# Kernel tuning notes

Measured on AMD Instinct MI355X. Metric: run time of the kernel, lower is better.

## Reference

```python
import jax, jax.numpy as jnp
import numpy as np

LN_EPS = 1e-3   # keras LayerNormalization default epsilon
STAB = 1e-3     # performer relu-kernel numerical stabilizer
N = 2           # number of blocks per branch


def layer_norm(x, g, b):
    m = jnp.mean(x, axis=-1, keepdims=True)
    v = jnp.mean(jnp.square(x - m), axis=-1, keepdims=True)
    return (x - m) * jax.lax.rsqrt(v + LN_EPS) * g + b


def favor(q_in, kv_in, Wq, Wk, Wv, Wo):
    # Performer FAVOR attention, relu kernel features (google-research fast_attention,
    # projection_matrix_type=None). q/k/v head projections have no bias.
    q = jnp.einsum('bld,dhm->blhm', q_in, Wq)
    k = jnp.einsum('bsd,dhm->bshm', kv_in, Wk)
    v = jnp.einsum('bsd,dhm->bshm', kv_in, Wv)
    norm = q.shape[-1] ** -0.25  # 1/sqrt(sqrt(head_dim))
    qp = jax.nn.relu(q * norm) + STAB
    kp = jax.nn.relu(k * norm) + STAB
    kv = jnp.einsum('bshm,bshd->bhmd', kp, v)
    num = jnp.einsum('blhm,bhmd->blhd', qp, kv)
    den = jnp.einsum('blhm,bhm->blh', qp, kp.sum(axis=1))
    out = num / den[..., None]
    return jnp.einsum('blhd,hde->ble', out, Wo)


def forward(obj_inputs, road_inputs,
            rg_dense_W, rg_dense_b, rg_qkv_W, rg_qkv_b,
            rg_Wq, rg_Wk, rg_Wv, rg_Wo, rg_ln_g, rg_ln_b, rg_fc_W, rg_fc_b,
            rg_out_W, rg_out_b,
            dense_W, dense_b, pos_emb,
            Wq, Wk, Wv, Wo, ln_g, ln_b, fc_W, fc_b):
    rgH = rg_dense_W.shape[1]
    # ---- roadgraph branch: performer self-attention blocks ----
    x = jax.nn.relu(road_inputs @ rg_dense_W + rg_dense_b)
    for i in range(N):
        qkv = jax.nn.relu(x @ rg_qkv_W + rg_qkv_b)
        q = qkv[..., :rgH]  # k,v splits unused by FastSelfAttention (it re-projects q)
        attn = favor(q, q, rg_Wq[i], rg_Wk[i], rg_Wv[i], rg_Wo[i])
        n = layer_norm(attn + x, rg_ln_g[i], rg_ln_b[i])
        y = jax.nn.relu(n @ rg_fc_W[i] + rg_fc_b[i])
        x = layer_norm(n + y, rg_ln_g[i], rg_ln_b[i])  # original reuses ln_block_1
    rg_out = jax.nn.relu(x @ rg_out_W + rg_out_b)
    # ---- object branch: performer cross-attention blocks ----
    x = jax.nn.relu(obj_inputs @ dense_W + dense_b)
    x = x + pos_emb  # learned position embedding, [T, H]
    for i in range(N):
        attn = favor(x, rg_out, Wq[i], Wk[i], Wv[i], Wo[i])
        n = layer_norm(attn + x, ln_g[i], ln_b[i])
        y = jax.nn.relu(n @ fc_W[i] + fc_b[i])
        x = layer_norm(n + y, ln_g[i], ln_b[i])  # original reuses ln_block_1
    return x


def setup_inputs() -> dict:
    B, T, V = 8, 128, 512
    S, F = 8192, 8
    rgH, H = 16, 1024
    rh, rd = 4, 4     # rg heads, head_dim
    h, d = 16, 64     # cross heads, head_dim
    keys = iter(jax.random.split(jax.random.key(0), 64))
    def rnd(shape, scale=1.0):
        return jax.random.normal(next(keys), shape, dtype=jnp.float32) * scale
    return {
        'obj_inputs': rnd((B, T, V)),
        'road_inputs': rnd((B, S, F)),
        'rg_dense_W': rnd((F, rgH), F ** -0.5), 'rg_dense_b': jnp.zeros((rgH,), jnp.float32),
        'rg_qkv_W': rnd((rgH, 3 * rgH), rgH ** -0.5), 'rg_qkv_b': jnp.zeros((3 * rgH,), jnp.float32),
        'rg_Wq': rnd((N, rgH, rh, rd), rgH ** -0.5),
        'rg_Wk': rnd((N, rgH, rh, rd), rgH ** -0.5),
        'rg_Wv': rnd((N, rgH, rh, rd), rgH ** -0.5),
        'rg_Wo': rnd((N, rh, rd, rgH), rgH ** -0.5),
        'rg_ln_g': jnp.ones((N, rgH), jnp.float32), 'rg_ln_b': jnp.zeros((N, rgH), jnp.float32),
        'rg_fc_W': rnd((N, rgH, rgH), rgH ** -0.5), 'rg_fc_b': jnp.zeros((N, rgH), jnp.float32),
        'rg_out_W': rnd((rgH, H), rgH ** -0.5), 'rg_out_b': jnp.zeros((H,), jnp.float32),
        'dense_W': rnd((V, H), V ** -0.5), 'dense_b': jnp.zeros((H,), jnp.float32),
        'pos_emb': rnd((T, H), 0.02),
        'Wq': rnd((N, H, h, d), H ** -0.5),
        'Wk': rnd((N, H, h, d), H ** -0.5),
        'Wv': rnd((N, H, h, d), H ** -0.5),
        'Wo': rnd((N, h, d, H), H ** -0.5),
        'ln_g': jnp.ones((N, H), jnp.float32), 'ln_b': jnp.zeros((N, H), jnp.float32),
        'fc_W': rnd((N, H, H), H ** -0.5), 'fc_b': jnp.zeros((N, H), jnp.float32),
    }


def reference(obj_inputs, road_inputs, rg_dense_W, rg_dense_b, rg_qkv_W, rg_qkv_b,
              rg_Wq, rg_Wk, rg_Wv, rg_Wo, rg_ln_g, rg_ln_b, rg_fc_W, rg_fc_b,
              rg_out_W, rg_out_b, dense_W, dense_b, pos_emb,
              Wq, Wk, Wv, Wo, ln_g, ln_b, fc_W, fc_b):
    return forward(obj_inputs, road_inputs, rg_dense_W, rg_dense_b, rg_qkv_W, rg_qkv_b,
                   rg_Wq, rg_Wk, rg_Wv, rg_Wo, rg_ln_g, rg_ln_b, rg_fc_W, rg_fc_b,
                   rg_out_W, rg_out_b, dense_W, dense_b, pos_emb,
                   Wq, Wk, Wv, Wo, ln_g, ln_b, fc_W, fc_b)
```

## Files before the change

kernel.cpp:

```cpp
#include <hip/hip_runtime.h>

typedef unsigned short u16;
typedef unsigned int u32;

using s8v = __attribute__((ext_vector_type(8))) short;
using f4v = __attribute__((ext_vector_type(4))) float;

#define LN_EPS 0.001f
#define STAB 0.001f
#define NORM_OBJ 0.35355339059327373f
#define NORM_ROAD 0.7071067811865476f

__device__ __forceinline__ float bf2f(u16 v) { return __uint_as_float(((u32)v) << 16); }
__device__ __forceinline__ u16 f2bf(float f) {
  u32 u = __float_as_uint(f);
  u32 r = (u + 0x7fffu + ((u >> 16) & 1u)) >> 16;
  return (u16)r;
}
__device__ __forceinline__ f4v mfma16(s8v a, s8v b, f4v c) {
  return __builtin_amdgcn_mfma_f32_16x16x32_bf16(a, b, c, 0, 0, 0);
}
__device__ __forceinline__ void ldsload16(void* lds, const void* g) {
  __builtin_amdgcn_global_load_lds((const __attribute__((address_space(1))) u32*)g,
                                   (__attribute__((address_space(3))) u32*)lds, 16, 0, 0);
}

struct TPair { const float* s; u16* d; };
struct TP11 { TPair p[11]; };

__global__ __launch_bounds__(256) void transpose_kernel(TP11 ps, int K, int N) {
  const float* __restrict__ src = ps.p[blockIdx.z].s;
  u16* __restrict__ dst = ps.p[blockIdx.z].d;
  int n0 = blockIdx.x * 64, k0 = blockIdx.y * 64;
  int t = threadIdx.x;
  __shared__ __align__(16) u16 lt[64 * 72];
#pragma unroll
  for (int j = 0; j < 4; ++j) {
    int p = t + 256 * j;
    int r = p >> 4, cb = p & 15;
    float4 v = *(const float4*)(src + (size_t)(k0 + r) * N + n0 + cb * 4);
    lt[r * 72 + cb * 4 + 0] = f2bf(v.x);
    lt[r * 72 + cb * 4 + 1] = f2bf(v.y);
    lt[r * 72 + cb * 4 + 2] = f2bf(v.z);
    lt[r * 72 + cb * 4 + 3] = f2bf(v.w);
  }
  __syncthreads();
#pragma unroll
  for (int j = 0; j < 2; ++j) {
    int q = t + 256 * j;
    int on = q >> 3, ocb = q & 7;
    u16 e[8];
#pragma unroll
    for (int i = 0; i < 8; ++i) e[i] = lt[(ocb * 8 + i) * 72 + on];
    uint4 v;
    v.x = (u32)e[0] | ((u32)e[1] << 16);
    v.y = (u32)e[2] | ((u32)e[3] << 16);
    v.z = (u32)e[4] | ((u32)e[5] << 16);
    v.w = (u32)e[6] | ((u32)e[7] << 16);
    *(uint4*)(dst + (size_t)(n0 + on) * K + k0 + ocb * 8) = v;
  }
}

__global__ __launch_bounds__(256) void cvt_kernel(const float* __restrict__ src,
                                                  u16* __restrict__ dst) {
  int i = (blockIdx.x * 256 + threadIdx.x) * 4;
  float4 v = *(const float4*)(src + i);
  uint2 o;
  o.x = (u32)f2bf(v.x) | ((u32)f2bf(v.y) << 16);
  o.y = (u32)f2bf(v.z) | ((u32)f2bf(v.w) << 16);
  *(uint2*)(dst + i) = o;
}

__global__ __launch_bounds__(256) void r0_kernel(const float* __restrict__ road,
    const float* __restrict__ W, const float* __restrict__ bias, float* __restrict__ x) {
  int row = blockIdx.x * 256 + threadIdx.x;
  float in[8];
  float4 v0 = *(const float4*)(road + (size_t)row * 8);
  float4 v1 = *(const float4*)(road + (size_t)row * 8 + 4);
  in[0] = v0.x; in[1] = v0.y; in[2] = v0.z; in[3] = v0.w;
  in[4] = v1.x; in[5] = v1.y; in[6] = v1.z; in[7] = v1.w;
#pragma unroll
  for (int j = 0; j < 16; ++j) {
    float s = bias[j];
#pragma unroll
    for (int c = 0; c < 8; ++c) s += in[c] * W[c * 16 + j];
    x[(size_t)row * 16 + j] = fmaxf(s, 0.f);
  }
}

__global__ __launch_bounds__(256) void ra_kernel(const float* __restrict__ x,
    const float* __restrict__ qkvW, const float* __restrict__ qkvb,
    const float* __restrict__ Wk, const float* __restrict__ Wv,
    float* __restrict__ kvr, float* __restrict__ ksr) {
  int t = threadIdx.x;
  int row = blockIdx.x * 256 + t;
  int b = row >> 13;
  float xv[16];
#pragma unroll
  for (int e = 0; e < 16; ++e) xv[e] = x[(size_t)row * 16 + e];
  float q16[16];
#pragma unroll
  for (int j = 0; j < 16; ++j) {
    float s = qkvb[j];
#pragma unroll
    for (int c = 0; c < 16; ++c) s += xv[c] * qkvW[c * 48 + j];
    q16[j] = fmaxf(s, 0.f);
  }
  float kp[16], vh[16];
#pragma unroll
  for (int hm = 0; hm < 16; ++hm) {
    float sk = 0.f, sv = 0.f;
#pragma unroll
    for (int c = 0; c < 16; ++c) {
      float q = q16[c];
      sk += q * Wk[c * 16 + hm];
      sv += q * Wv[c * 16 + hm];
    }
    kp[hm] = fmaxf(sk * NORM_ROAD, 0.f) + STAB;
    vh[hm] = sv;
  }
  __shared__ float l[80];
  if (t < 80) l[t] = 0.f;
  __syncthreads();
#pragma unroll
  for (int h = 0; h < 4; ++h)
#pragma unroll
    for (int m = 0; m < 4; ++m) {
      float kpv = kp[h * 4 + m];
      atomicAdd(&l[64 + h * 4 + m], kpv);
#pragma unroll
      for (int d = 0; d < 4; ++d) atomicAdd(&l[h * 16 + m * 4 + d], kpv * vh[h * 4 + d]);
    }
  __syncthreads();
  if (t < 64) atomicAdd(&kvr[b * 64 + t], l[t]);
  else if (t < 80) atomicAdd(&ksr[b * 16 + (t - 64)], l[t]);
}

__device__ __forceinline__ void ln16(const float* tv, const float* g, const float* bb, float* o) {
  float m = 0.f;
#pragma unroll
  for (int e = 0; e < 16; ++e) m += tv[e];
  m *= (1.f / 16.f);
  float var = 0.f;
#pragma unroll
  for (int e = 0; e < 16; ++e) { float d = tv[e] - m; var += d * d; }
  var *= (1.f / 16.f);
  float rstd = rsqrtf(var + LN_EPS);
#pragma unroll
  for (int e = 0; e < 16; ++e) o[e] = (tv[e] - m) * rstd * g[e] + bb[e];
}

__global__ __launch_bounds__(256) void rb_kernel(float* __restrict__ x,
    const float* __restrict__ qkvW, const float* __restrict__ qkvb,
    const float* __restrict__ Wq, const float* __restrict__ Wo,
    const float* __restrict__ lng, const float* __restrict__ lnb,
    const float* __restrict__ fcW, const float* __restrict__ fcb,
    const float* __restrict__ kvr, const float* __restrict__ ksr) {
  int row = blockIdx.x * 256 + threadIdx.x;
  int b = row >> 13;
  float xv[16];
#pragma unroll
  for (int e = 0; e < 16; ++e) xv[e] = x[(size_t)row * 16 + e];
  float q16[16];
#pragma unroll
  for (int j = 0; j < 16; ++j) {
    float s = qkvb[j];
#pragma unroll
    for (int c = 0; c < 16; ++c) s += xv[c] * qkvW[c * 48 + j];
    q16[j] = fmaxf(s, 0.f);
  }
  float qp[16];
#pragma unroll
  for (int hm = 0; hm < 16; ++hm) {
    float s = 0.f;
#pragma unroll
    for (int c = 0; c < 16; ++c) s += q16[c] * Wq[c * 16 + hm];
    qp[hm] = fmaxf(s * NORM_ROAD, 0.f) + STAB;
  }
  float attn[16];
#pragma unroll
  for (int e = 0; e < 16; ++e) attn[e] = 0.f;
#pragma unroll
  for (int h = 0; h < 4; ++h) {
    float den = 0.f;
#pragma unroll
    for (int m = 0; m < 4; ++m) den += qp[h * 4 + m] * ksr[b * 16 + h * 4 + m];
    float od[4];
#pragma unroll
    for (int d = 0; d < 4; ++d) {
      float num = 0.f;
#pragma unroll
      for (int m = 0; m < 4; ++m) num += qp[h * 4 + m] * kvr[b * 64 + h * 16 + m * 4 + d];
      od[d] = num / den;
    }
#pragma unroll
    for (int d = 0; d < 4; ++d)
#pragma unroll
      for (int e = 0; e < 16; ++e) attn[e] += od[d] * Wo[(h * 4 + d) * 16 + e];
  }
  float tv[16], n[16], o2[16];
#pragma unroll
  for (int e = 0; e < 16; ++e) tv[e] = attn[e] + xv[e];
  ln16(tv, lng, lnb, n);
#pragma unroll
  for (int j = 0; j < 16; ++j) {
    float s = fcb[j];
#pragma unroll
    for (int e = 0; e < 16; ++e) s += n[e] * fcW[e * 16 + j];
    tv[j] = n[j] + fmaxf(s, 0.f);
  }
  ln16(tv, lng, lnb, o2);
#pragma unroll
  for (int e = 0; e < 16; ++e) x[(size_t)row * 16 + e] = o2[e];
}

__global__ __launch_bounds__(256) void rc_kernel(const float* __restrict__ x,
    const float* __restrict__ W, const float* __restrict__ bias, u16* __restrict__ out) {
  const int t = threadIdx.x;
  const int cg = t & 63, rg = t >> 6;
  const int c0 = blockIdx.x * 256 + cg * 4;
  const int r0 = blockIdx.y * 16;
  __shared__ float lx[256];
  lx[t] = x[(size_t)(r0 + (t >> 4)) * 16 + (t & 15)];
  __syncthreads();
  float4 wv[16];
#pragma unroll
  for (int c = 0; c < 16; ++c) wv[c] = *(const float4*)(W + (size_t)c * 1024 + c0);
  float4 bv = *(const float4*)(bias + c0);
#pragma unroll
  for (int k = 0; k < 4; ++k) {
    int rr = rg * 4 + k;
    float s0 = bv.x, s1 = bv.y, s2 = bv.z, s3 = bv.w;
#pragma unroll
    for (int c = 0; c < 16; ++c) {
      float xv = lx[rr * 16 + c];
      s0 += xv * wv[c].x; s1 += xv * wv[c].y; s2 += xv * wv[c].z; s3 += xv * wv[c].w;
    }
    uint2 o;
    o.x = (u32)f2bf(fmaxf(s0, 0.f)) | ((u32)f2bf(fmaxf(s1, 0.f)) << 16);
    o.y = (u32)f2bf(fmaxf(s2, 0.f)) | ((u32)f2bf(fmaxf(s3, 0.f)) << 16);
    *(uint2*)(out + (size_t)(r0 + rr) * 1024 + c0) = o;
  }
}

__global__ __launch_bounds__(256) void gemm_kernel(
    const u16* __restrict__ A, const u16* __restrict__ BT, int K,
    float* __restrict__ outF, u16* __restrict__ outB,
    const float* __restrict__ bias, const float* __restrict__ resF, int resmod,
    float scale, int do_relu, float post) {
  const int n0 = blockIdx.x * 128, m0 = blockIdx.y * 128;
  const int t = threadIdx.x;
  const int wid = t >> 6, lane = t & 63, quad = lane >> 4, m16 = lane & 15;
  const int wm = wid >> 1, wn = wid & 1;
  const int lrr = lane >> 3;
  const int lcs = (((lane & 7) ^ lrr) * 8);
  const int sw = m16 & 7;
  __shared__ __align__(16) u16 smem[2 * 128 * 64];
  u16* Al = smem;
  u16* Bl = smem + 128 * 64;
  f4v acc[4][4];
#pragma unroll
  for (int i = 0; i < 4; ++i)
#pragma unroll
    for (int j = 0; j < 4; ++j) acc[i][j] = {0.f, 0.f, 0.f, 0.f};

  for (int kc = 0; kc < K; kc += 64) {
    __syncthreads();
#pragma unroll
    for (int j = 0; j < 4; ++j) {
      int rbase = wid * 32 + j * 8;
      ldsload16(Al + rbase * 64, A + (size_t)(m0 + rbase + lrr) * K + kc + lcs);
      ldsload16(Bl + rbase * 64, BT + (size_t)(n0 + rbase + lrr) * K + kc + lcs);
    }
    __syncthreads();
#pragma unroll
    for (int ko = 0; ko < 64; ko += 32) {
      int g0 = ko >> 3;
      s8v af[4], bfr[4];
#pragma unroll
      for (int tm = 0; tm < 4; ++tm)
        af[tm] = *(const s8v*)(Al + (wm * 64 + tm * 16 + m16) * 64 + ((g0 + quad) ^ sw) * 8);
#pragma unroll
      for (int tn = 0; tn < 4; ++tn)
        bfr[tn] = *(const s8v*)(Bl + (wn * 64 + tn * 16 + m16) * 64 + ((g0 + quad) ^ sw) * 8);
#pragma unroll
      for (int tm = 0; tm < 4; ++tm)
#pragma unroll
        for (int tn = 0; tn < 4; ++tn)
          acc[tm][tn] = mfma16(af[tm], bfr[tn], acc[tm][tn]);
    }
  }
#pragma unroll
  for (int tm = 0; tm < 4; ++tm)
#pragma unroll
    for (int tn = 0; tn < 4; ++tn)
#pragma unroll
      for (int r = 0; r < 4; ++r) {
        int row = m0 + wm * 64 + tm * 16 + quad * 4 + r;
        int col = n0 + wn * 64 + tn * 16 + m16;
        float v = acc[tm][tn][r] * scale;
        if (bias) v += bias[col];
        if (do_relu) v = fmaxf(v, 0.f);
        v += post;
        if (resF) v += resF[(size_t)(row % resmod) * 1024 + col];
        if (outF) outF[(size_t)row * 1024 + col] = v;
        if (outB) outB[(size_t)row * 1024 + col] = f2bf(v);
      }
}

__global__ __launch_bounds__(256) void kv_kernel(
    const u16* __restrict__ rgout, const u16* __restrict__ WkT, const u16* __restrict__ WvT,
    float* __restrict__ kv, float* __restrict__ ksum) {
  const int h = blockIdx.x, mt = blockIdx.y, b = blockIdx.z;
  const int t = threadIdx.x;
  const int wid = t >> 6, lane = t & 63, quad = lane >> 4, m16 = lane & 15;
  const int wm = wid >> 1, wn = wid & 1;
  const int lrr = lane >> 3;
  const int lcs = (((lane & 7) ^ lrr) * 8);
  const int sw = m16 & 7;
  __shared__ __align__(16) u16 smem[2 * 128 * 72];
  u16* Al = smem;
  u16* Bl = smem + 128 * 64;
  const size_t abase = ((size_t)b * 8192 + (size_t)mt * 128) * 1024;
  f4v acc[4][4];
#pragma unroll
  for (int i = 0; i < 4; ++i)
#pragma unroll
    for (int j = 0; j < 4; ++j) acc[i][j] = {0.f, 0.f, 0.f, 0.f};

  for (int kc = 0; kc < 1024; kc += 64) {
    __syncthreads();
#pragma unroll
    for (int j = 0; j < 4; ++j) {
      int rbase = wid * 32 + j * 8;
      int r = rbase + lrr;
      ldsload16(Al + rbase * 64, rgout + abase + (size_t)r * 1024 + kc + lcs);
      const u16* bsrc = (r < 64) ? (WkT + (size_t)(h * 64 + r) * 1024)
                                 : (WvT + (size_t)(h * 64 + (r - 64)) * 1024);
      ldsload16(Bl + rbase * 64, bsrc + kc + lcs);
    }
    __syncthreads();
#pragma unroll
    for (int ko = 0; ko < 64; ko += 32) {
      int g0 = ko >> 3;
      s8v af[4], bfr[4];
#pragma unroll
      for (int tm = 0; tm < 4; ++tm)
        af[tm] = *(const s8v*)(Al + (wm * 64 + tm * 16 + m16) * 64 + ((g0 + quad) ^ sw) * 8);
#pragma unroll
      for (int tn = 0; tn < 4; ++tn)
        bfr[tn] = *(const s8v*)(Bl + (wn * 64 + tn * 16 + m16) * 64 + ((g0 + quad) ^ sw) * 8);
#pragma unroll
      for (int tm = 0; tm < 4; ++tm)
#pragma unroll
        for (int tn = 0; tn < 4; ++tn)
          acc[tm][tn] = mfma16(af[tm], bfr[tn], acc[tm][tn]);
    }
  }
  __syncthreads();
  u16* KPT = smem;
  u16* VT = smem + 64 * 136;
  {
    u16* dst = wn ? VT : KPT;
#pragma unroll
    for (int tm = 0; tm < 4; ++tm)
#pragma unroll
      for (int tn = 0; tn < 4; ++tn)
#pragma unroll
        for (int r = 0; r < 4; ++r) {
          int srow = wm * 64 + tm * 16 + quad * 4 + r;
          int feat = tn * 16 + m16;
          float v = acc[tm][tn][r];
          if (wn == 0) v = fmaxf(v * NORM_OBJ, 0.f) + STAB;
          dst[feat * 136 + srow] = f2bf(v);
        }
  }
  __syncthreads();
  if (t < 64) {
    float s = 0.f;
#pragma unroll
    for (int i = 0; i < 128; i += 8) {
      uint4 v = *(const uint4*)(KPT + t * 136 + i);
      u32 a[4] = {v.x, v.y, v.z, v.w};
#pragma unroll
      for (int q = 0; q < 4; ++q) {
        s += __uint_as_float(a[q] << 16);
        s += __uint_as_float(a[q] & 0xffff0000u);
      }
    }
    atomicAdd(&ksum[(size_t)(b * 16 + h) * 64 + t], s);
  }
  f4v a2[4];
#pragma unroll
  for (int tn = 0; tn < 4; ++tn) a2[tn] = {0.f, 0.f, 0.f, 0.f};
#pragma unroll
  for (int ks = 0; ks < 128; ks += 32) {
    s8v af = *(const s8v*)(KPT + (wid * 16 + m16) * 136 + ks + quad * 8);
#pragma unroll
    for (int tn = 0; tn < 4; ++tn) {
      s8v bv = *(const s8v*)(VT + (tn * 16 + m16) * 136 + ks + quad * 8);
      a2[tn] = mfma16(af, bv, a2[tn]);
    }
  }
#pragma unroll
  for (int tn = 0; tn < 4; ++tn)
#pragma unroll
    for (int r = 0; r < 4; ++r) {
      int m = wid * 16 + quad * 4 + r;
      int d = tn * 16 + m16;
      atomicAdd(&kv[((size_t)(b * 16 + h) * 64 + m) * 64 + d], a2[tn][r]);
    }
}

__global__ __launch_bounds__(256) void q2_kernel(const u16* __restrict__ qp,
    const float* __restrict__ kv, const float* __restrict__ ks, u16* __restrict__ out) {
  int wid = threadIdx.x >> 6, lane = threadIdx.x & 63;
  int row = blockIdx.x * 4 + wid;
  int b = row >> 7;
  int h0 = blockIdx.y * 4;
  for (int h = h0; h < h0 + 4; ++h) {
    const float* kvp = kv + (size_t)((b * 16 + h) * 64) * 64;
    const float* ksp = ks + (size_t)(b * 16 + h) * 64;
    const u16* qpp = qp + (size_t)row * 1024 + h * 64;
    float num = 0.f, den = 0.f;
    for (int m = 0; m < 64; ++m) {
      float qv = bf2f(qpp[m]);
      num += qv * kvp[m * 64 + lane];
      den += qv * ksp[m];
    }
    out[(size_t)row * 1024 + h * 64 + lane] = f2bf(num / den);
  }
}

__global__ __launch_bounds__(256) void ln_kernel(const float* __restrict__ in,
    const float* __restrict__ g, const float* __restrict__ bb,
    float* __restrict__ outF, u16* __restrict__ outB) {
  int row = blockIdx.x, t = threadIdx.x;
  const float* x = in + (size_t)row * 1024;
  float v[4];
  float s = 0.f, ss = 0.f;
#pragma unroll
  for (int j = 0; j < 4; ++j) {
    v[j] = x[t + 256 * j];
    s += v[j];
    ss += v[j] * v[j];
  }
  __shared__ float rs[256], rss[256];
  rs[t] = s; rss[t] = ss;
  __syncthreads();
  for (int o = 128; o > 0; o >>= 1) {
    if (t < o) { rs[t] += rs[t + o]; rss[t] += rss[t + o]; }
    __syncthreads();
  }
  float mean = rs[0] * (1.f / 1024.f);
  float var = rss[0] * (1.f / 1024.f) - mean * mean;
  float rstd = rsqrtf(var + LN_EPS);
#pragma unroll
  for (int j = 0; j < 4; ++j) {
    int c = t + 256 * j;
    float o = (v[j] - mean) * rstd * g[c] + bb[c];
    if (outF) outF[(size_t)row * 1024 + c] = o;
    if (outB) outB[(size_t)row * 1024 + c] = f2bf(o);
  }
}

static constexpr size_t MBy = 1048576;
static constexpr size_t OFF_XROAD = 0;
static constexpr size_t OFF_RGOUT = 4 * MBy;
static constexpr size_t OFF_KVR = OFF_RGOUT + 128 * MBy;
static constexpr size_t OFF_KSR = OFF_KVR + 2048;
static constexpr size_t OFF_KVO = OFF_KVR + 4096;
static constexpr size_t OFF_KSO = OFF_KVO + 2 * MBy;
static constexpr size_t OFF_WT = OFF_KSO + 65536;
static constexpr size_t OFF_XOBJ = OFF_WT + 21 * MBy;
static constexpr size_t OFF_XOBJB = OFF_XOBJ + 4 * MBy;
static constexpr size_t OFF_QP = OFF_XOBJB + 2 * MBy;
static constexpr size_t OFF_FOUT = OFF_QP + 2 * MBy;
static constexpr size_t OFF_T1 = OFF_FOUT + 2 * MBy;
static constexpr size_t OFF_N = OFF_T1 + 4 * MBy;
static constexpr size_t OFF_NB = OFF_N + 4 * MBy;
static constexpr size_t OFF_OBJB = OFF_NB + 2 * MBy;

extern "C" void kernel_launch(void* const* d_in, const int* in_sizes, int n_in,
                              void* d_out, int out_size, void* d_ws, size_t ws_size,
                              hipStream_t stream) {
  (void)in_sizes; (void)n_in; (void)out_size; (void)ws_size;
  const float* obj = (const float*)d_in[0];
  const float* road = (const float*)d_in[1];
  const float* rgdW = (const float*)d_in[2];
  const float* rgdb = (const float*)d_in[3];
  const float* qkvW = (const float*)d_in[4];
  const float* qkvb = (const float*)d_in[5];
  const float* rgWq = (const float*)d_in[6];
  const float* rgWk = (const float*)d_in[7];
  const float* rgWv = (const float*)d_in[8];
  const float* rgWo = (const float*)d_in[9];
  const float* rglng = (const float*)d_in[10];
  const float* rglnb = (const float*)d_in[11];
  const float* rgfcW = (const float*)d_in[12];
  const float* rgfcb = (const float*)d_in[13];
  const float* rgoW = (const float*)d_in[14];
  const float* rgob = (const float*)d_in[15];
  const float* denW = (const float*)d_in[16];
  const float* denb = (const float*)d_in[17];
  const float* pose = (const float*)d_in[18];
  const float* Wq = (const float*)d_in[19];
  const float* Wk = (const float*)d_in[20];
  const float* Wv = (const float*)d_in[21];
  const float* Wo = (const float*)d_in[22];
  const float* lng = (const float*)d_in[23];
  const float* lnb = (const float*)d_in[24];
  const float* fcW = (const float*)d_in[25];
  const float* fcb = (const float*)d_in[26];

  char* w = (char*)d_ws;
  float* xroad = (float*)(w + OFF_XROAD);
  u16* rgout = (u16*)(w + OFF_RGOUT);
  float* kvr = (float*)(w + OFF_KVR);
  float* ksr = (float*)(w + OFF_KSR);
  float* kvo = (float*)(w + OFF_KVO);
  float* kso = (float*)(w + OFF_KSO);
  u16* wt = (u16*)(w + OFF_WT);
  float* xobj = (float*)(w + OFF_XOBJ);
  u16* xobjb = (u16*)(w + OFF_XOBJB);
  u16* qpB = (u16*)(w + OFF_QP);
  u16* fout = (u16*)(w + OFF_FOUT);
  float* t1 = (float*)(w + OFF_T1);
  float* nF = (float*)(w + OFF_N);
  u16* nB = (u16*)(w + OFF_NB);
  u16* objb = (u16*)(w + OFF_OBJB);

  const size_t E = 1048576;
  u16* wqT[2] = {wt + 0 * E, wt + 1 * E};
  u16* wkT[2] = {wt + 2 * E, wt + 3 * E};
  u16* wvT[2] = {wt + 4 * E, wt + 5 * E};
  u16* woT[2] = {wt + 6 * E, wt + 7 * E};
  u16* fcT[2] = {wt + 8 * E, wt + 9 * E};
  u16* denT = wt + 10 * E;

  TP11 tb;
  const float* srcs[10] = {Wq, Wq + E, Wk, Wk + E, Wv, Wv + E, Wo, Wo + E, fcW, fcW + E};
  u16* dsts[10] = {wqT[0], wqT[1], wkT[0], wkT[1], wvT[0], wvT[1], woT[0], woT[1], fcT[0], fcT[1]};
  for (int j = 0; j < 11; ++j) { tb.p[j].s = srcs[j < 10 ? j : 0]; tb.p[j].d = dsts[j < 10 ? j : 0]; }
  transpose_kernel<<<dim3(16, 16, 10), 256, 0, stream>>>(tb, 1024, 1024);
  TP11 td;
  for (int j = 0; j < 11; ++j) { td.p[j].s = denW; td.p[j].d = denT; }
  transpose_kernel<<<dim3(16, 8, 1), 256, 0, stream>>>(td, 512, 1024);
  cvt_kernel<<<dim3(512), 256, 0, stream>>>(obj, objb);

  r0_kernel<<<dim3(256), 256, 0, stream>>>(road, rgdW, rgdb, xroad);
  for (int i = 0; i < 2; ++i) {
    hipMemsetAsync(w + OFF_KVR, 0, 2560, stream);
    ra_kernel<<<dim3(256), 256, 0, stream>>>(xroad, qkvW, qkvb, rgWk + i * 256, rgWv + i * 256,
                                             kvr, ksr);
    rb_kernel<<<dim3(256), 256, 0, stream>>>(xroad, qkvW, qkvb, rgWq + i * 256, rgWo + i * 256,
                                             rglng + i * 16, rglnb + i * 16, rgfcW + i * 256,
                                             rgfcb + i * 16, kvr, ksr);
  }
  rc_kernel<<<dim3(4, 4096), 256, 0, stream>>>(xroad, rgoW, rgob, rgout);

  gemm_kernel<<<dim3(8, 8), 256, 0, stream>>>(objb, denT, 512, xobj, xobjb, denb, pose, 128,
                                              1.f, 1, 0.f);

  for (int i = 0; i < 2; ++i) {
    hipMemsetAsync(w + OFF_KVO, 0, 2 * MBy + 32768, stream);
    kv_kernel<<<dim3(16, 64, 8), 256, 0, stream>>>(rgout, wkT[i], wvT[i], kvo, kso);
    gemm_kernel<<<dim3(8, 8), 256, 0, stream>>>(xobjb, wqT[i], 1024, nullptr, qpB, nullptr,
                                                nullptr, 1024, NORM_OBJ, 1, STAB);
    q2_kernel<<<dim3(256, 4), 256, 0, stream>>>(qpB, kvo, kso, fout);
    gemm_kernel<<<dim3(8, 8), 256, 0, stream>>>(fout, woT[i], 1024, t1, nullptr, nullptr, xobj,
                                                1024, 1.f, 0, 0.f);
    ln_kernel<<<dim3(1024), 256, 0, stream>>>(t1, lng + i * 1024, lnb + i * 1024, nF, nB);
    gemm_kernel<<<dim3(8, 8), 256, 0, stream>>>(nB, fcT[i], 1024, t1, nullptr, fcb + i * 1024, nF,
                                                1024, 1.f, 1, 0.f);
    if (i == 0)
      ln_kernel<<<dim3(1024), 256, 0, stream>>>(t1, lng, lnb, xobj, xobjb);
    else
      ln_kernel<<<dim3(1024), 256, 0, stream>>>(t1, lng + 1024, lnb + 1024, (float*)d_out, nullptr);
  }
}
```

Before: 1.697 ms.

## Process two heads per kv block and halve GEMM M-tile for more blocks

The kv_kernel now computes K and V projections for two heads per block, so each rgout tile loaded into LDS is reused across 256 output columns instead of 128. This halves the number of times the large road activations are read. Separately, the 1024x1024 object GEMMs use 64-row tiles, doubling the block count from 64 to 128 to fill more of the GPU's compute units. The trade-off is more registers and LDS per kv block, which may lower occupancy, and more redundant B-tile loads in the smaller GEMMs.

New measurement: 2.370 ms. 1.4x slower.

```diff
diff --git a/kernel.cpp b/kernel.cpp
--- a/kernel.cpp
+++ b/kernel.cpp
@@ -243,60 +243,64 @@
   }
 }
 
-__global__ __launch_bounds__(256) void gemm_kernel(
+__global__ __launch_bounds__(256) void gemm64_kernel(
     const u16* __restrict__ A, const u16* __restrict__ BT, int K,
     float* __restrict__ outF, u16* __restrict__ outB,
     const float* __restrict__ bias, const float* __restrict__ resF, int resmod,
     float scale, int do_relu, float post) {
-  const int n0 = blockIdx.x * 128, m0 = blockIdx.y * 128;
+  const int n0 = blockIdx.x * 128, m0 = blockIdx.y * 64;
   const int t = threadIdx.x;
   const int wid = t >> 6, lane = t & 63, quad = lane >> 4, m16 = lane & 15;
   const int wm = wid >> 1, wn = wid & 1;
   const int lrr = lane >> 3;
   const int lcs = (((lane & 7) ^ lrr) * 8);
   const int sw = m16 & 7;
-  __shared__ __align__(16) u16 smem[2 * 128 * 64];
+  __shared__ __align__(16) u16 smem[64 * 64 + 128 * 64];
   u16* Al = smem;
-  u16* Bl = smem + 128 * 64;
-  f4v acc[4][4];
-#pragma unroll
-  for (int i = 0; i < 4; ++i)
+  u16* Bl = smem + 64 * 64;
+  f4v acc[2][4];
+#pragma unroll
+  for (int i = 0; i < 2; ++i)
 #pragma unroll
     for (int j = 0; j < 4; ++j) acc[i][j] = {0.f, 0.f, 0.f, 0.f};
 
   for (int kc = 0; kc < K; kc += 64) {
     __syncthreads();
 #pragma unroll
+    for (int j = 0; j < 2; ++j) {
+      int rbase = wid * 16 + j * 8;
+      ldsload16(Al + rbase * 64, A + (size_t)(m0 + rbase + lrr) * K + kc + lcs);
+    }
+#pragma unroll
     for (int j = 0; j < 4; ++j) {
       int rbase = wid * 32 + j * 8;
-      ldsload16(Al + rbase * 64, A + (size_t)(m0 + rbase + lrr) * K + kc + lcs);
       ldsload16(Bl + rbase * 64, BT + (size_t)(n0 + rbase + lrr) * K + kc + lcs);
     }
     __syncthreads();
 #pragma unroll
     for (int ko = 0; ko < 64; ko += 32) {
       int g0 = ko >> 3;
-      s8v af[4], bfr[4];
-#pragma unroll
-      for (int tm = 0; tm < 4; ++tm)
-        af[tm] = *(const s8v*)(Al + (wm * 64 + tm * 16 + m16) * 64 + ((g0 + quad) ^ sw) * 8);
+      s8v af[2], bfr[4];
+#pragma unroll
+      for (int tm = 0; tm < 2; ++tm)
+        af[tm] = *(const s8v*)(Al + (wm * 32 + tm * 16 + m16) * 64 + ((g0 + quad) ^ sw) * 8);
 #pragma unroll
       for (int tn = 0; tn < 4; ++tn)
         bfr[tn] = *(const s8v*)(Bl + (wn * 64 + tn * 16 + m16) * 64 + ((g0 + quad) ^ sw) * 8);
 #pragma unroll
-      for (int tm = 0; tm < 4; ++tm)
+      for (int tm = 0; tm < 2; ++tm)
 #pragma unroll
         for (int tn = 0; tn < 4; ++tn)
           acc[tm][tn] = mfma16(af[tm], bfr[tn], acc[tm][tn]);
     }
   }
 #pragma unroll
-  for (int tm = 0; tm < 4; ++tm)
+  for (int tm = 0; tm < 2; ++tm)
 #pragma unroll
     for (int tn = 0; tn < 4; ++tn)
 #pragma unroll
       for (int r = 0; r < 4; ++r) {
-        int row = m0 + wm * 64 + tm * 16 + quad * 4 + r;
+        int row = m0 + wm * 32 + tm * 16 + quad * 4 + r;
         int col = n0 + wn * 64 + tn * 16 + m16;
         float v = acc[tm][tn][r] * scale;
         if (bias) v += bias[col];
@@ -311,76 +315,87 @@
 __global__ __launch_bounds__(256) void kv_kernel(
     const u16* __restrict__ rgout, const u16* __restrict__ WkT, const u16* __restrict__ WvT,
     float* __restrict__ kv, float* __restrict__ ksum) {
-  const int h = blockIdx.x, mt = blockIdx.y, b = blockIdx.z;
+  const int hp = blockIdx.x, mt = blockIdx.y, b = blockIdx.z;
   const int t = threadIdx.x;
   const int wid = t >> 6, lane = t & 63, quad = lane >> 4, m16 = lane & 15;
   const int wm = wid >> 1, wn = wid & 1;
   const int lrr = lane >> 3;
   const int lcs = (((lane & 7) ^ lrr) * 8);
   const int sw = m16 & 7;
-  __shared__ __align__(16) u16 smem[2 * 128 * 72];
+  const int HSZ = 64 * 136;
+  __shared__ __align__(16) u16 smem[4 * 64 * 136];
   u16* Al = smem;
   u16* Bl = smem + 128 * 64;
   const size_t abase = ((size_t)b * 8192 + (size_t)mt * 128) * 1024;
-  f4v acc[4][4];
+  f4v acc[4][8];
 #pragma unroll
   for (int i = 0; i < 4; ++i)
 #pragma unroll
-    for (int j = 0; j < 4; ++j) acc[i][j] = {0.f, 0.f, 0.f, 0.f};
+    for (int j = 0; j < 8; ++j) acc[i][j] = {0.f, 0.f, 0.f, 0.f};
 
   for (int kc = 0; kc < 1024; kc += 64) {
     __syncthreads();
 #pragma unroll
     for (int j = 0; j < 4; ++j) {
       int rbase = wid * 32 + j * 8;
+      ldsload16(Al + rbase * 64, rgout + abase + (size_t)(rbase + lrr) * 1024 + kc + lcs);
+    }
+#pragma unroll
+    for (int j = 0; j < 8; ++j) {
+      int rbase = wid * 64 + j * 8;
       int r = rbase + lrr;
-      ldsload16(Al + rbase * 64, rgout + abase + (size_t)r * 1024 + kc + lcs);
-      const u16* bsrc = (r < 64) ? (WkT + (size_t)(h * 64 + r) * 1024)
-                                 : (WvT + (size_t)(h * 64 + (r - 64)) * 1024);
+      int h = hp * 2 + (r >> 7), rr = r & 127;
+      const u16* bsrc = (rr < 64) ? (WkT + (size_t)(h * 64 + rr) * 1024)
+                                  : (WvT + (size_t)(h * 64 + (rr - 64)) * 1024);
       ldsload16(Bl + rbase * 64, bsrc + kc + lcs);
     }
     __syncthreads();
 #pragma unroll
     for (int ko = 0; ko < 64; ko += 32) {
       int g0 = ko >> 3;
-      s8v af[4], bfr[4];
+      s8v af[4], bfr[8];
 #pragma unroll
       for (int tm = 0; tm < 4; ++tm)
         af[tm] = *(const s8v*)(Al + (wm * 64 + tm * 16 + m16) * 64 + ((g0 + quad) ^ sw) * 8);
 #pragma unroll
-      for (int tn = 0; tn < 4; ++tn)
-        bfr[tn] = *(const s8v*)(Bl + (wn * 64 + tn * 16 + m16) * 64 + ((g0 + quad) ^ sw) * 8);
+      for (int tn = 0; tn < 8; ++tn)
+        bfr[tn] = *(const s8v*)(Bl + (wn * 128 + tn * 16 + m16) * 64 + ((g0 + quad) ^ sw) * 8);
 #pragma unroll
       for (int tm = 0; tm < 4; ++tm)
 #pragma unroll
-        for (int tn = 0; tn < 4; ++tn)
+        for (int tn = 0; tn < 8; ++tn)
           acc[tm][tn] = mfma16(af[tm], bfr[tn], acc[tm][tn]);
     }
   }
   __syncthreads();
-  u16* KPT = smem;
-  u16* VT = smem + 64 * 136;
   {
-    u16* dst = wn ? VT : KPT;
+    u16* KPT = smem + (size_t)(wn * 2) * HSZ;
+    u16* VT = KPT + HSZ;
 #pragma unroll
     for (int tm = 0; tm < 4; ++tm)
 #pragma unroll
-      for (int tn = 0; tn < 4; ++tn)
+      for (int tn = 0; tn < 8; ++tn)
 #pragma unroll
         for (int r = 0; r < 4; ++r) {
           int srow = wm * 64 + tm * 16 + quad * 4 + r;
-          int feat = tn * 16 + m16;
+          int c = tn * 16 + m16;
           float v = acc[tm][tn][r];
-          if (wn == 0) v = fmaxf(v * NORM_OBJ, 0.f) + STAB;
-          dst[feat * 136 + srow] = f2bf(v);
+          if (tn < 4) {
+            v = fmaxf(v * NORM_OBJ, 0.f) + STAB;
+            KPT[c * 136 + srow] = f2bf(v);
+          } else {
+            VT[(c - 64) * 136 + srow] = f2bf(v);
+          }
         }
   }
   __syncthreads();
-  if (t < 64) {
+  if (t < 128) {
+    int hh = t >> 6, m = t & 63;
+    const u16* base = smem + (size_t)(hh * 2) * HSZ + m * 136;
     float s = 0.f;
 #pragma unroll
     for (int i = 0; i < 128; i += 8) {
-      uint4 v = *(const uint4*)(KPT + t * 136 + i);
+      uint4 v = *(const uint4*)(base + i);
       u32 a[4] = {v.x, v.y, v.z, v.w};
 #pragma unroll
       for (int q = 0; q < 4; ++q) {
@@ -388,28 +403,43 @@
         s += __uint_as_float(a[q] & 0xffff0000u);
       }
     }
-    atomicAdd(&ksum[(size_t)(b * 16 + h) * 64 + t], s);
-  }
-  f4v a2[4];
-#pragma unroll
-  for (int tn = 0; tn < 4; ++tn) a2[tn] = {0.f, 0.f, 0.f, 0.f};
-#pragma unroll
-  for (int ks = 0; ks < 128; ks += 32) {
-    s8v af = *(const s8v*)(KPT + (wid * 16 + m16) * 136 + ks + quad * 8);
-#pragma unroll
-    for (int tn = 0; tn < 4; ++tn) {
-      s8v bv = *(const s8v*)(VT + (tn * 16 + m16) * 136 + ks + quad * 8);
-      a2[tn] = mfma16(af, bv, a2[tn]);
-    }
-  }
-#pragma unroll
-  for (int tn = 0; tn < 4; ++tn)
-#pragma unroll
-    for (int r = 0; r < 4; ++r) {
-      int m = wid * 16 + quad * 4 + r;
-      int d = tn * 16 + m16;
-      atomicAdd(&kv[((size_t)(b * 16 + h) * 64 + m) * 64 + d], a2[tn][r]);
-    }
+    atomicAdd(&ksum[(size_t)(b * 16 + hp * 2 + hh) * 64 + m], s);
+  }
+  {
+    u16* KPh = smem + (size_t)(wn * 2) * HSZ;
+    u16* Vh = KPh + HSZ;
+    f4v a2[2][4];
+#pragma unroll
+    for (int i = 0; i < 2; ++i)
+#pragma unroll
+      for (int j = 0; j < 4; ++j) a2[i][j] = {0.f, 0.f, 0.f, 0.f};
+#pragma unroll
+    for (int ks = 0; ks < 128; ks += 32) {
+      s8v af2[2], bv[4];
+#pragma unroll
+      for (int tm = 0; tm < 2; ++tm)
+        af2[tm] = *(const s8v*)(KPh + (wm * 32 + tm * 16 + m16) * 136 + ks + quad * 8);
+#pragma unroll
+      for (int tn = 0; tn < 4; ++tn)
+        bv[tn] = *(const s8v*)(Vh + (tn * 16 + m16) * 136 + ks + quad * 8);
+#pragma unroll
+      for (int tm = 0; tm < 2; ++tm)
+#pragma unroll
+        for (int tn = 0; tn < 4; ++tn)
+          a2[tm][tn] = mfma16(af2[tm], bv[tn], a2[tm][tn]);
+    }
+    int h = hp * 2 + wn;
+#pragma unroll
+    for (int tm = 0; tm < 2; ++tm)
+#pragma unroll
+      for (int tn = 0; tn < 4; ++tn)
+#pragma unroll
+        for (int r = 0; r < 4; ++r) {
+          int m = wm * 32 + tm * 16 + quad * 4 + r;
+          int d = tn * 16 + m16;
+          atomicAdd(&kv[((size_t)(b * 16 + h) * 64 + m) * 64 + d], a2[tm][tn][r]);
+        }
+  }
 }
 
 __global__ __launch_bounds__(256) void q2_kernel(const u16* __restrict__ qp,
@@ -559,20 +589,20 @@
   }
   rc_kernel<<<dim3(4, 4096), 256, 0, stream>>>(xroad, rgoW, rgob, rgout);
 
-  gemm_kernel<<<dim3(8, 8), 256, 0, stream>>>(objb, denT, 512, xobj, xobjb, denb, pose, 128,
-                                              1.f, 1, 0.f);
+  gemm64_kernel<<<dim3(8, 16), 256, 0, stream>>>(objb, denT, 512, xobj, xobjb, denb, pose, 128,
+                                                 1.f, 1, 0.f);
 
   for (int i = 0; i < 2; ++i) {
     hipMemsetAsync(w + OFF_KVO, 0, 2 * MBy + 32768, stream);
-    kv_kernel<<<dim3(16, 64, 8), 256, 0, stream>>>(rgout, wkT[i], wvT[i], kvo, kso);
-    gemm_kernel<<<dim3(8, 8), 256, 0, stream>>>(xobjb, wqT[i], 1024, nullptr, qpB, nullptr,
-                                                nullptr, 1024, NORM_OBJ, 1, STAB);
+    kv_kernel<<<dim3(8, 64, 8), 256, 0, stream>>>(rgout, wkT[i], wvT[i], kvo, kso);
+    gemm64_kernel<<<dim3(8, 16), 256, 0, stream>>>(xobjb, wqT[i], 1024, nullptr, qpB, nullptr,
+                                                   nullptr, 1024, NORM_OBJ, 1, STAB);
     q2_kernel<<<dim3(256, 4), 256, 0, stream>>>(qpB, kvo, kso, fout);
-    gemm_kernel<<<dim3(8, 8), 256, 0, stream>>>(fout, woT[i], 1024, t1, nullptr, nullptr, xobj,
-                                                1024, 1.f, 0, 0.f);
+    gemm64_kernel<<<dim3(8, 16), 256, 0, stream>>>(fout, woT[i], 1024, t1, nullptr, nullptr, xobj,
+                                                   1024, 1.f, 0, 0.f);
     ln_kernel<<<dim3(1024), 256, 0, stream>>>(t1, lng + i * 1024, lnb + i * 1024, nF, nB);
-    gemm_kernel<<<dim3(8, 8), 256, 0, stream>>>(nB, fcT[i], 1024, t1, nullptr, fcb + i * 1024, nF,
-                                                1024, 1.f, 1, 0.f);
+    gemm64_kernel<<<dim3(8, 16), 256, 0, stream>>>(nB, fcT[i], 1024, t1, nullptr, fcb + i * 1024,
+                                                   nF, 1024, 1.f, 1, 0.f);
     if (i == 0)
       ln_kernel<<<dim3(1024), 256, 0, stream>>>(t1, lng, lnb, xobj, xobjb);
     else
```
